# Kernel optimization log

Measured on AMD Instinct MI355X. Metric: run time of the kernel, lower is better.

## Reference

```python
import jax, jax.numpy as jnp
import numpy as np

MIN_BIN_W = 1e-3
MIN_BIN_H = 1e-3
MIN_DERIV = 1e-3
EPS = 1e-6


def _mlp(x, W0, b0, W1, b1, W2, b2):
    h = jax.nn.relu(x @ W0 + b0)
    h = jax.nn.relu(h @ W1 + b1)
    return h @ W2 + b2


def _rqs_forward(inputs, widths, heights, derivatives):
    # inputs: [B, D]; widths/heights: [B, D, nb]; derivatives: [B, D, nb-1]
    nb = widths.shape[-1]
    inputs = jnp.clip(inputs, 0.0, 1.0)
    widths = jax.nn.softmax(widths, axis=-1)
    heights = jax.nn.softmax(heights, axis=-1)
    widths = MIN_BIN_W + (1.0 - MIN_BIN_W * nb) * widths
    heights = MIN_BIN_H + (1.0 - MIN_BIN_H * nb) * heights
    derivatives = jax.nn.softplus(derivatives) + MIN_DERIV

    pad2 = [(0, 0), (0, 0)]
    x_knots = jnp.pad(jnp.cumsum(widths, axis=-1), pad2 + [(1, 0)])   # [B,D,nb+1]
    y_knots = jnp.pad(jnp.cumsum(heights, axis=-1), pad2 + [(1, 0)])
    derivs = jnp.pad(derivatives, pad2 + [(1, 1)], constant_values=1.0)  # [B,D,nb+1]

    # searchsorted (side='left'): count of knots strictly less than input
    bin_idx = jnp.sum(x_knots < inputs[..., None], axis=-1)
    bin_idx = jnp.clip(bin_idx, 1, nb)[..., None]  # [B,D,1]

    g = lambda a, i: jnp.take_along_axis(a, i, axis=-1)[..., 0]
    x_k = g(x_knots, bin_idx - 1)
    y_k = g(y_knots, bin_idx - 1)
    w_k = g(widths, bin_idx - 1)
    h_k = g(heights, bin_idx - 1)
    d_k = g(derivs, bin_idx - 1)
    d_k1 = g(derivs, bin_idx)

    s_k = h_k / w_k
    theta = (inputs - x_k) / w_k
    t1t = theta * (1.0 - theta)
    den = s_k + (d_k + d_k1 - 2.0 * s_k) * t1t
    outputs = y_k + h_k * (s_k * theta ** 2 + d_k * t1t) / (den + EPS)
    nom_d = s_k ** 2 * (d_k1 * theta ** 2 + 2.0 * s_k * t1t + d_k * (1.0 - theta) ** 2)
    log_det = jnp.log(nom_d / (den ** 2 + EPS))
    return outputs, log_det


def setup_inputs() -> dict:
    key = jax.random.key(0)
    ks = jax.random.split(key, 7)
    B, D, H, NB = 65536, 64, 512, 8
    out_dim = D * (3 * NB - 1)
    inp = {
        "x": jax.random.uniform(ks[0], (B, D), dtype=jnp.float32),
        "W0": jax.random.normal(ks[1], (D, H), dtype=jnp.float32) * 0.05,
        "b0": jnp.zeros((H,), jnp.float32),
        "W1": jax.random.normal(ks[2], (H, H), dtype=jnp.float32) * 0.05,
        "b1": jnp.zeros((H,), jnp.float32),
        "W2": jax.random.normal(ks[3], (H, out_dim), dtype=jnp.float32) * 0.05,
        "b2": jnp.zeros((out_dim,), jnp.float32),
        "num_bins": NB,
    }
    return inp


def reference(x, W0, b0, W1, b1, W2, b2, num_bins):
    B, D = x.shape
    nb = int(num_bins)
    params = _mlp(x, W0, b0, W1, b1, W2, b2).reshape(B, D, 3 * nb - 1)
    widths = params[..., :nb]
    heights = params[..., nb:2 * nb]
    derivatives = params[..., 2 * nb:]
    z, log_det = _rqs_forward(x, widths, heights, derivatives)
    return z, jnp.sum(log_det, axis=1)
```

## Files before the change

### kernel.cpp

```cpp
#include <hip/hip_runtime.h>

typedef unsigned short u16;
typedef __bf16 bf16x8 __attribute__((ext_vector_type(8)));
typedef float f32x4 __attribute__((ext_vector_type(4)));

__device__ __forceinline__ u16 f2bf_r(float f) {
    union { float f; unsigned u; } v; v.f = f;
    return (u16)((v.u + 0x8000u) >> 16);
}
__device__ __forceinline__ float rcpf(float x) { return __builtin_amdgcn_rcpf(x); }

__device__ __forceinline__ void gload_lds16(const u16* g, u16* l) {
    __builtin_amdgcn_global_load_lds(
        (const __attribute__((address_space(1))) void*)g,
        (__attribute__((address_space(3))) void*)l,
        16, 0, 0);
}


#define BM 128
#define BN 128
#define BK 32

template<int K, int RELU, int NBX>
__global__ __launch_bounds__(256) void gemm_bt(
    const u16* __restrict__ A, const u16* __restrict__ BT,
    const float* __restrict__ bias, u16* __restrict__ C,
    int M, int N)
{
    constexpr int NS = K / BK;
    __shared__ u16 smem[3 * 8192];
    const int t = threadIdx.x;
    const int lane = t & 63;
    const int wave = t >> 6;
    const int wr = (wave >> 1) * 64;
    const int wc = (wave & 1) * 64;

    const int nlin = blockIdx.x;
    const int jj = nlin >> 3;
    const long brow = (long)((nlin & 7) + 8 * (jj / NBX)) * BM;
    const long bcol = (long)(jj % NBX) * BN;

    const int sr = t >> 2;
    const int sc = ((t & 3) ^ ((t >> 3) & 3)) * 8;
    const u16* gA0 = A + (brow + sr) * (long)K + sc;
    const u16* gA1 = gA0 + 64L * K;
    const u16* gB0 = BT + (bcol + sr) * (long)K + sc;
    const u16* gB1 = gB0 + 64L * K;

    f32x4 acc[4][4] = {};
    const int fr = lane & 15;
    const int fbase = fr * 32 + (((lane >> 4) ^ ((fr >> 1) & 3)) * 8);

    auto STAGE = [&](int buf, int k0) {
        u16* As = &smem[buf * 8192];
        u16* Bs = As + 4096;
        gload_lds16(gA0 + k0, &As[t * 8]);
        gload_lds16(gA1 + k0, &As[2048 + t * 8]);
        gload_lds16(gB0 + k0, &Bs[t * 8]);
        gload_lds16(gB1 + k0, &Bs[2048 + t * 8]);
    };
    auto COMPUTE = [&](int buf) {
        const u16* As = &smem[buf * 8192];
        const u16* Bs = As + 4096;
        bf16x8 af[4], bfr[4];
#pragma unroll
        for (int m = 0; m < 4; ++m)
            af[m] = *(const bf16x8*)&As[wr * 32 + m * 512 + fbase];
#pragma unroll
        for (int n = 0; n < 4; ++n)
            bfr[n] = *(const bf16x8*)&Bs[wc * 32 + n * 512 + fbase];
#pragma unroll
        for (int m = 0; m < 4; ++m)
#pragma unroll
            for (int n = 0; n < 4; ++n)
                acc[m][n] = __builtin_amdgcn_mfma_f32_16x16x32_bf16(
                    af[m], bfr[n], acc[m][n], 0, 0, 0);
    };

    STAGE(0, 0);
    STAGE(1, BK);
#pragma unroll
    for (int i = 0; i < NS; ++i) {
        if (i < NS - 1) asm volatile("s_waitcnt vmcnt(4)" ::: "memory");
        else            asm volatile("s_waitcnt vmcnt(0)" ::: "memory");
        __builtin_amdgcn_s_barrier();
        __builtin_amdgcn_sched_barrier(0);
        if (i + 2 < NS) STAGE((i + 2) % 3, (i + 2) * BK);
        COMPUTE(i % 3);
    }

#pragma unroll
    for (int n = 0; n < 4; ++n) {
        const long col = bcol + wc + n * 16 + fr;
        const float bv = bias[col];
#pragma unroll
        for (int m = 0; m < 4; ++m) {
            const long row = brow + wr + m * 16 + (lane >> 4) * 4;
#pragma unroll
            for (int j = 0; j < 4; ++j) {
                float v = acc[m][n][j] + bv;
                if (RELU) v = fmaxf(v, 0.f);
                C[(row + j) * (long)N + col] = f2bf_r(v);
            }
        }
    }
}

#define FBM 128
#define FBN 192
#define FBK 32
#define CLS 200

template<int K>
__global__ __launch_bounds__(256) void gemm3_rqs(
    const u16* __restrict__ A,
    const u16* __restrict__ BT,
    const float* __restrict__ bias,
    const float* __restrict__ x,
    float* __restrict__ z,
    float* __restrict__ ldp8)
{
    constexpr int NS = K / FBK;
    __shared__ u16 smem[3 * 10240];
    const int t = threadIdx.x;
    const int lane = t & 63;
    const int wave = t >> 6;
    const int wr = (wave >> 1) * 64;
    const int wc = (wave & 1) * 96;

    const int nlin = blockIdx.x;
    const int jj = nlin >> 3;
    const long brow = (long)((nlin & 7) + 8 * (jj >> 3)) * FBM;
    const int bx = jj & 7;
    const int bcol = bx * FBN;

    const int sr = t >> 2;
    const int sc = ((t & 3) ^ ((t >> 3) & 3)) * 8;
    const u16* gA0 = A + (brow + sr) * (long)K + sc;
    const u16* gB0 = BT + (long)(bcol + sr) * K + sc;

    f32x4 acc[4][6] = {};
    const int fr = lane & 15;
    const int gsel = ((lane >> 4) ^ ((fr >> 1) & 3)) * 8;
    const int fbase = fr * 32 + gsel;

    int b_off[6];
#pragma unroll
    for (int n = 0; n < 6; ++n) {
        int rb = wc + n * 16 + fr;
        b_off[n] = (rb >> 6) * 2048 + (rb & 63) * 32 + gsel;
    }

    auto STAGE = [&](int buf, int k0) {
        u16* As = &smem[buf * 10240];
        u16* Bs = As + 4096;
        gload_lds16(gA0 + k0,            &As[t * 8]);
        gload_lds16(gA0 + 64L * K + k0,  &As[2048 + t * 8]);
        gload_lds16(gB0 + k0,            &Bs[t * 8]);
        gload_lds16(gB0 + 64L * K + k0,  &Bs[2048 + t * 8]);
        gload_lds16(gB0 + 128L * K + k0, &Bs[4096 + t * 8]);
    };
    auto COMPUTE = [&](int buf) {
        const u16* As = &smem[buf * 10240];
        const u16* Bs = As + 4096;
        bf16x8 af[4], bfr[6];
#pragma unroll
        for (int m = 0; m < 4; ++m)
            af[m] = *(const bf16x8*)&As[wr * 32 + m * 512 + fbase];
#pragma unroll
        for (int n = 0; n < 6; ++n)
            bfr[n] = *(const bf16x8*)&Bs[b_off[n]];
#pragma unroll
        for (int m = 0; m < 4; ++m)
#pragma unroll
            for (int n = 0; n < 6; ++n)
                acc[m][n] = __builtin_amdgcn_mfma_f32_16x16x32_bf16(
                    af[m], bfr[n], acc[m][n], 0, 0, 0);
    };

    STAGE(0, 0);
    STAGE(1, FBK);
#pragma unroll
    for (int i = 0; i < NS; ++i) {
        if (i < NS - 1) asm volatile("s_waitcnt vmcnt(5)" ::: "memory");
        else            asm volatile("s_waitcnt vmcnt(0)" ::: "memory");
        __builtin_amdgcn_s_barrier();
        __builtin_amdgcn_sched_barrier(0);
        if (i + 2 < NS) STAGE((i + 2) % 3, (i + 2) * FBK);
        COMPUTE(i % 3);
    }
    __syncthreads();

#pragma unroll
    for (int n = 0; n < 6; ++n) {
        const int cl = wc + n * 16 + fr;
        const float bv = bias[bcol + cl];
#pragma unroll
        for (int m = 0; m < 4; ++m) {
            const int rl = wr + m * 16 + (lane >> 4) * 4;
#pragma unroll
            for (int j = 0; j < 4; ++j)
                smem[(rl + j) * CLS + cl] = f2bf_r(acc[m][n][j] + bv);
        }
    }
    __syncthreads();

    const int dbase = bx * 8;
#pragma unroll
    for (int pi = 0; pi < 4; ++pi) {
        const int p  = t + pi * 256;
        const int bl = p >> 3;
        const int dl = p & 7;
        const u16* pp = &smem[bl * CLS + dl * 24];
        bf16x8 v0 = *(const bf16x8*)(pp);
        bf16x8 v1 = *(const bf16x8*)(pp + 8);
        bf16x8 v2 = *(const bf16x8*)(pp + 16);

        float w[8], h[8];
        float sw = 0.f, sh = 0.f;
#pragma unroll
        for (int i = 0; i < 8; ++i) { w[i] = __expf((float)v0[i]); sw += w[i]; }
#pragma unroll
        for (int i = 0; i < 8; ++i) { h[i] = __expf((float)v1[i]); sh += h[i]; }
        const float rw = 0.992f * rcpf(sw);
        const float rh = 0.992f * rcpf(sh);
#pragma unroll
        for (int i = 0; i < 8; ++i) w[i] = fmaf(w[i], rw, 0.001f);
#pragma unroll
        for (int i = 0; i < 8; ++i) h[i] = fmaf(h[i], rh, 0.001f);

        const long b = brow + bl;
        const int  d = dbase + dl;
        float xin = x[b * 64 + d];
        xin = fminf(fmaxf(xin, 0.f), 1.f);

        float x_k = 0.f, y_k = 0.f, w_k = w[0], h_k = h[0];
        float rk = 0.f, rk1 = (float)v2[0];
        bool isfirst = true, islast = false;
        float cw = 0.f, ch = 0.f;
#pragma unroll
        for (int i = 1; i < 8; ++i) {
            cw += w[i - 1]; ch += h[i - 1];
            if (cw < xin) {
                x_k = cw; y_k = ch; w_k = w[i]; h_k = h[i];
                rk = (float)v2[i - 1];
                rk1 = (i < 7) ? (float)v2[i] : 0.f;
                isfirst = false; islast = (i == 7);
            }
        }
        float sp_k  = __logf(1.f + __expf(rk));
        float sp_k1 = __logf(1.f + __expf(rk1));
        float d_k  = isfirst ? 1.f : sp_k  + 0.001f;
        float d_k1 = islast  ? 1.f : sp_k1 + 0.001f;

        const float inv_wk = rcpf(w_k);
        const float s   = h_k * inv_wk;
        const float th  = (xin - x_k) * inv_wk;
        const float omt = 1.f - th;
        const float t1t = th * omt;
        const float den = fmaf(d_k + d_k1 - 2.f * s, t1t, s);
        const float num = fmaf(s * th, th, d_k * t1t);
        const float out = fmaf(h_k * num, rcpf(den + 1e-6f), y_k);
        const float nom = s * s * fmaf(d_k1 * th, th, fmaf(2.f * s, t1t, d_k * omt * omt));
        const float logdet = __logf(nom) - __logf(fmaf(den, den, 1e-6f));

        z[b * 64 + d] = out;

        float r = logdet;
        r += __shfl_xor(r, 1, 64);
        r += __shfl_xor(r, 2, 64);
        r += __shfl_xor(r, 4, 64);
        if ((t & 7) == 0) ldp8[b * 8 + bx] = r;
    }
}

__global__ __launch_bounds__(256) void ld_reduce8(
    const float* __restrict__ ldp8, float* __restrict__ ld)
{
    const long b = (long)blockIdx.x * 256 + threadIdx.x;
    const f32x4 a = *(const f32x4*)&ldp8[b * 8];
    const f32x4 c = *(const f32x4*)&ldp8[b * 8 + 4];
    ld[b] = ((a[0] + a[1]) + (a[2] + a[3])) + ((c[0] + c[1]) + (c[2] + c[3]));
}

__global__ __launch_bounds__(256) void prep_all(
    const float* __restrict__ x,  u16* __restrict__ xb,
    const float* __restrict__ W0, u16* __restrict__ W0T,
    const float* __restrict__ W1, u16* __restrict__ W1T,
    const float* __restrict__ W2, u16* __restrict__ W2T,
    const float* __restrict__ b2, float* __restrict__ b2p)
{
    const int bid = blockIdx.x;
    const int t = threadIdx.x;
    if (bid < 2048) {
        const long i8 = ((long)bid * 256 + t) * 8;
        const f32x4 v0 = *(const f32x4*)&x[i8];
        const f32x4 v1 = *(const f32x4*)&x[i8 + 4];
        u16 o[8];
#pragma unroll
        for (int j = 0; j < 4; ++j) o[j] = f2bf_r(v0[j]);
#pragma unroll
        for (int j = 0; j < 4; ++j) o[4 + j] = f2bf_r(v1[j]);
        *(ulong2*)&xb[i8] = *(const ulong2*)o;
    } else if (bid < 2176) {
        const int i = (bid - 2048) * 256 + t;
        const int n = i >> 6, k = i & 63;
        W0T[i] = f2bf_r(W0[k * 512 + n]);
    } else if (bid < 3200) {
        const int i = (bid - 2176) * 256 + t;
        const int n = i >> 9, k = i & 511;
        W1T[i] = f2bf_r(W1[k * 512 + n]);
    } else if (bid < 6272) {
        const int i = (bid - 3200) * 256 + t;
        const int npad = i >> 9, k = i & 511;
        const int g = npad / 24, r = npad % 24;
        float v = (r < 23) ? W2[(long)k * 1472 + g * 23 + r] : 0.f;
        W2T[i] = f2bf_r(v);
    } else {
        const int c = (bid - 6272) * 256 + t;
        if (c < 1536) {
            const int g = c / 24, r = c % 24;
            b2p[c] = (r < 23) ? b2[g * 23 + r] : 0.f;
        }
    }
}

__global__ void fill_fail(float* __restrict__ out, long n) {
    long i = (long)blockIdx.x * blockDim.x + threadIdx.x;
    long stride = (long)gridDim.x * blockDim.x;
    for (; i < n; i += stride) out[i] = -1.0f;
}

extern "C" void kernel_launch(void* const* d_in, const int* in_sizes, int n_in,
                              void* d_out, int out_size, void* d_ws, size_t ws_size,
                              hipStream_t stream)
{
    const float* x  = (const float*)d_in[0];
    const float* W0 = (const float*)d_in[1];
    const float* b0 = (const float*)d_in[2];
    const float* W1 = (const float*)d_in[3];
    const float* b1 = (const float*)d_in[4];
    const float* W2 = (const float*)d_in[5];
    const float* b2 = (const float*)d_in[6];
    const int B = in_sizes[0] / 64;
    const int D = 64, H = 512, NP = 1536;

    char* ws = (char*)d_ws;
    size_t off = 0;
    u16* W0T = (u16*)(ws + off); off += (size_t)H * D * 2;
    u16* W1T = (u16*)(ws + off); off += (size_t)H * H * 2;
    u16* W2T = (u16*)(ws + off); off += (size_t)NP * H * 2;
    float* b2p = (float*)(ws + off); off += (size_t)NP * 4;
    off = (off + 255) & ~(size_t)255;
    u16*   h1   = (u16*)(ws + off);
    float* ldp8 = (float*)(ws + off);
    off += (size_t)B * H * 2;
    u16* xb = (u16*)(ws + off);
    u16* h2 = (u16*)(ws + off);
    off += (size_t)B * H * 2;
    size_t need = off;

    float* zout  = (float*)d_out;
    float* ldout = zout + (size_t)B * D;

    if (ws_size < need) {
        fill_fail<<<2048, 256, 0, stream>>>(zout, (long)out_size);
        return;
    }

    prep_all<<<6278, 256, 0, stream>>>(x, xb, W0, W0T, W1, W1T, W2, W2T, b2, b2p);

    gemm_bt<64, 1, 4><<<2048, 256, 0, stream>>>(xb, W0T, b0, h1, B, H);
    gemm_bt<512, 1, 4><<<2048, 256, 0, stream>>>(h1, W1T, b1, h2, B, H);

    gemm3_rqs<512><<<4096, 256, 0, stream>>>(h2, W2T, b2p, x, zout, ldp8);

    ld_reduce8<<<B / 256, 256, 0, stream>>>(ldp8, ldout);
}
```

Before: 198.1 us.

## Tile weight transposes through LDS and raise wave priority around MFMA blocks

The weight transpose/convert section of the prep kernel now stages 128x128 (or 128x64) tiles in padded shared memory. Reads are coalesced along n and writes go out as 8-byte stores along k, replacing one-element-per-thread strided transposes and cutting the block count. Separately, both GEMM compute lambdas wrap their MFMA loops in s_setprio(1)/s_setprio(0) so waves doing matrix math get issue priority over waves issuing loads. The LDS tile adds shared memory to every prep block, including the x-conversion blocks, which may lower occupancy there.

```diff
diff --git a/kernel.cpp b/kernel.cpp
--- a/kernel.cpp
+++ b/kernel.cpp
@@ -70,12 +70,14 @@
 #pragma unroll
         for (int n = 0; n < 4; ++n)
             bfr[n] = *(const bf16x8*)&Bs[wc * 32 + n * 512 + fbase];
+        __builtin_amdgcn_s_setprio(1);
 #pragma unroll
         for (int m = 0; m < 4; ++m)
 #pragma unroll
             for (int n = 0; n < 4; ++n)
                 acc[m][n] = __builtin_amdgcn_mfma_f32_16x16x32_bf16(
                     af[m], bfr[n], acc[m][n], 0, 0, 0);
+        __builtin_amdgcn_s_setprio(0);
     };
 
     STAGE(0, 0);
@@ -171,12 +173,14 @@
 #pragma unroll
         for (int n = 0; n < 6; ++n)
             bfr[n] = *(const bf16x8*)&Bs[b_off[n]];
+        __builtin_amdgcn_s_setprio(1);
 #pragma unroll
         for (int m = 0; m < 4; ++m)
 #pragma unroll
             for (int n = 0; n < 6; ++n)
                 acc[m][n] = __builtin_amdgcn_mfma_f32_16x16x32_bf16(
                     af[m], bfr[n], acc[m][n], 0, 0, 0);
+        __builtin_amdgcn_s_setprio(0);
     };
 
     STAGE(0, 0);
@@ -291,8 +295,10 @@
     const float* __restrict__ W2, u16* __restrict__ W2T,
     const float* __restrict__ b2, float* __restrict__ b2p)
 {
+    __shared__ u16 lds[128 * 132];
     const int bid = blockIdx.x;
     const int t = threadIdx.x;
+
     if (bid < 2048) {
         const long i8 = ((long)bid * 256 + t) * 8;
         const f32x4 v0 = *(const f32x4*)&x[i8];
@@ -303,22 +309,58 @@
 #pragma unroll
         for (int j = 0; j < 4; ++j) o[4 + j] = f2bf_r(v1[j]);
         *(ulong2*)&xb[i8] = *(const ulong2*)o;
-    } else if (bid < 2176) {
-        const int i = (bid - 2048) * 256 + t;
-        const int n = i >> 6, k = i & 63;
-        W0T[i] = f2bf_r(W0[k * 512 + n]);
-    } else if (bid < 3200) {
-        const int i = (bid - 2176) * 256 + t;
-        const int n = i >> 9, k = i & 511;
-        W1T[i] = f2bf_r(W1[k * 512 + n]);
-    } else if (bid < 6272) {
-        const int i = (bid - 3200) * 256 + t;
-        const int npad = i >> 9, k = i & 511;
-        const int g = npad / 24, r = npad % 24;
-        float v = (r < 23) ? W2[(long)k * 1472 + g * 23 + r] : 0.f;
-        W2T[i] = f2bf_r(v);
+    } else if (bid < 2052) {
+        const int n0 = (bid - 2048) * 128;
+#pragma unroll
+        for (int rr = 0; rr < 32; ++rr) {
+            const int idx = rr * 256 + t;
+            const int nl = idx & 127, k = idx >> 7;
+            lds[nl * 68 + k] = f2bf_r(W0[k * 512 + n0 + nl]);
+        }
+        __syncthreads();
+        const int nl = t >> 1, k0 = (t & 1) * 32;
+#pragma unroll
+        for (int j = 0; j < 8; ++j) {
+            ulong v = *(const ulong*)&lds[nl * 68 + k0 + j * 4];
+            *(ulong*)&W0T[(long)(n0 + nl) * 64 + k0 + j * 4] = v;
+        }
+    } else if (bid < 2068) {
+        const int tile = bid - 2052;
+        const int k0t = (tile >> 2) * 128, n0 = (tile & 3) * 128;
+#pragma unroll
+        for (int rr = 0; rr < 64; ++rr) {
+            const int idx = rr * 256 + t;
+            const int nl = idx & 127, k = idx >> 7;
+            lds[nl * 132 + k] = f2bf_r(W1[(long)(k0t + k) * 512 + n0 + nl]);
+        }
+        __syncthreads();
+        const int nl = t >> 1, k0 = (t & 1) * 64;
+#pragma unroll
+        for (int j = 0; j < 16; ++j) {
+            ulong v = *(const ulong*)&lds[nl * 132 + k0 + j * 4];
+            *(ulong*)&W1T[(long)(n0 + nl) * 512 + k0t + k0 + j * 4] = v;
+        }
+    } else if (bid < 2116) {
+        const int tile = bid - 2068;
+        const int k0t = (tile / 12) * 128, n0 = (tile % 12) * 128;
+#pragma unroll
+        for (int rr = 0; rr < 64; ++rr) {
+            const int idx = rr * 256 + t;
+            const int nl = idx & 127, k = idx >> 7;
+            const int npad = n0 + nl;
+            const int g = npad / 24, r = npad % 24;
+            float v = (r < 23) ? W2[(long)(k0t + k) * 1472 + g * 23 + r] : 0.f;
+            lds[nl * 132 + k] = f2bf_r(v);
+        }
+        __syncthreads();
+        const int nl = t >> 1, k0 = (t & 1) * 64;
+#pragma unroll
+        for (int j = 0; j < 16; ++j) {
+            ulong v = *(const ulong*)&lds[nl * 132 + k0 + j * 4];
+            *(ulong*)&W2T[(long)(n0 + nl) * 512 + k0t + k0 + j * 4] = v;
+        }
     } else {
-        const int c = (bid - 6272) * 256 + t;
+        const int c = (bid - 2116) * 256 + t;
         if (c < 1536) {
             const int g = c / 24, r = c % 24;
             b2p[c] = (r < 23) ? b2[g * 23 + r] : 0.f;
@@ -369,7 +411,7 @@
         return;
     }
 
-    prep_all<<<6278, 256, 0, stream>>>(x, xb, W0, W0T, W1, W1T, W2, W2T, b2, b2p);
+    prep_all<<<2122, 256, 0, stream>>>(x, xb, W0, W0T, W1, W1T, W2, W2T, b2, b2p);
 
     gemm_bt<64, 1, 4><<<2048, 256, 0, stream>>>(xb, W0T, b0, h1, B, H);
     gemm_bt<512, 1, 4><<<2048, 256, 0, stream>>>(h1, W1T, b1, h2, B, H);
```

Result: slower. 212.4 us (+7.2%).

## Load B fragments directly from global into registers, double-buffered

Applied to the files above, without the earlier changes.

The fused third GEMM no longer stages the B (weight) tile through LDS. Each lane now loads its MFMA B fragments straight from global memory into a two-set register buffer, one k-step ahead. Only A still uses the triple-buffered global_load_lds path, and shared memory is sized for the epilogue tile. This is meant to cut LDS traffic and footprint for B. In exchange it adds strided global reads that rely on cache hits, and the loop drops its explicit vmcnt wait before the barrier, so visibility of the staged A tile rests on compiler-inserted waits.

```diff
diff --git a/kernel.cpp b/kernel.cpp
--- a/kernel.cpp
+++ b/kernel.cpp
@@ -122,7 +122,7 @@
     float* __restrict__ ldp8)
 {
     constexpr int NS = K / FBK;
-    __shared__ u16 smem[3 * 10240];
+    __shared__ u16 smem[FBM * CLS];
     const int t = threadIdx.x;
     const int lane = t & 63;
     const int wave = t >> 6;
@@ -138,57 +138,55 @@
     const int sr = t >> 2;
     const int sc = ((t & 3) ^ ((t >> 3) & 3)) * 8;
     const u16* gA0 = A + (brow + sr) * (long)K + sc;
-    const u16* gB0 = BT + (long)(bcol + sr) * K + sc;
 
     f32x4 acc[4][6] = {};
     const int fr = lane & 15;
     const int gsel = ((lane >> 4) ^ ((fr >> 1) & 3)) * 8;
     const int fbase = fr * 32 + gsel;
 
-    int b_off[6];
-#pragma unroll
-    for (int n = 0; n < 6; ++n) {
-        int rb = wc + n * 16 + fr;
-        b_off[n] = (rb >> 6) * 2048 + (rb & 63) * 32 + gsel;
-    }
+    const u16* gBb = BT + (long)(bcol + wc + fr) * K + (lane >> 4) * 8;
 
     auto STAGE = [&](int buf, int k0) {
-        u16* As = &smem[buf * 10240];
-        u16* Bs = As + 4096;
-        gload_lds16(gA0 + k0,            &As[t * 8]);
-        gload_lds16(gA0 + 64L * K + k0,  &As[2048 + t * 8]);
-        gload_lds16(gB0 + k0,            &Bs[t * 8]);
-        gload_lds16(gB0 + 64L * K + k0,  &Bs[2048 + t * 8]);
-        gload_lds16(gB0 + 128L * K + k0, &Bs[4096 + t * 8]);
-    };
-    auto COMPUTE = [&](int buf) {
-        const u16* As = &smem[buf * 10240];
-        const u16* Bs = As + 4096;
-        bf16x8 af[4], bfr[6];
+        u16* As = &smem[buf * 4096];
+        gload_lds16(gA0 + k0,           &As[t * 8]);
+        gload_lds16(gA0 + 64L * K + k0, &As[2048 + t * 8]);
+    };
+
+    bf16x8 regB[2][6];
+    auto LOADB = [&](int set, int k0) {
+#pragma unroll
+        for (int n = 0; n < 6; ++n)
+            regB[set][n] = *(const bf16x8*)&gBb[n * 16 * K + k0];
+    };
+    auto COMPUTE = [&](int buf, int set) {
+        const u16* As = &smem[buf * 4096];
+        bf16x8 af[4];
 #pragma unroll
         for (int m = 0; m < 4; ++m)
             af[m] = *(const bf16x8*)&As[wr * 32 + m * 512 + fbase];
 #pragma unroll
-        for (int n = 0; n < 6; ++n)
-            bfr[n] = *(const bf16x8*)&Bs[b_off[n]];
-#pragma unroll
         for (int m = 0; m < 4; ++m)
 #pragma unroll
             for (int n = 0; n < 6; ++n)
                 acc[m][n] = __builtin_amdgcn_mfma_f32_16x16x32_bf16(
-                    af[m], bfr[n], acc[m][n], 0, 0, 0);
+                    af[m], regB[set][n], acc[m][n], 0, 0, 0);
     };
 
     STAGE(0, 0);
     STAGE(1, FBK);
+    LOADB(0, 0);
+    asm volatile("s_waitcnt vmcnt(8)" ::: "memory");
+    __builtin_amdgcn_s_barrier();
+    __builtin_amdgcn_sched_barrier(0);
+
 #pragma unroll
     for (int i = 0; i < NS; ++i) {
-        if (i < NS - 1) asm volatile("s_waitcnt vmcnt(5)" ::: "memory");
-        else            asm volatile("s_waitcnt vmcnt(0)" ::: "memory");
+        if (i + 2 < NS) STAGE((i + 2) % 3, (i + 2) * FBK);
+        if (i + 1 < NS) LOADB((i + 1) & 1, (i + 1) * FBK);
+        COMPUTE(i % 3, i & 1);
+        __builtin_amdgcn_sched_barrier(0);
         __builtin_amdgcn_s_barrier();
         __builtin_amdgcn_sched_barrier(0);
-        if (i + 2 < NS) STAGE((i + 2) % 3, (i + 2) * FBK);
-        COMPUTE(i % 3);
     }
     __syncthreads();
 
```

Result: slower. 295.2 us (+49.0%).
